# Performance work log

Measured on AMD Instinct MI355X. Metric: run time of the kernel, lower is better.

## Reference

```python
import jax, jax.numpy as jnp
import numpy as np

NUM_HEADS = 8


def setup_inputs() -> dict:
    key = jax.random.key(0)
    B, T, N, C = 16, 24, 716, 256
    H = NUM_HEADS
    D = C // H
    ks = jax.random.split(key, 14)

    def w(k, shape, scale=0.02):
        return jax.random.normal(k, shape, dtype=jnp.float32) * scale

    return {
        "x": jax.random.normal(ks[0], (B, T, N, C), dtype=jnp.float32),
        # nn.Linear weights stored PyTorch-style [out, in]
        "Wq": w(ks[1], (C, C)), "bq": w(ks[2], (C,)),
        "Wk": w(ks[3], (C, C)), "bk": w(ks[4], (C,)),
        "Wv": w(ks[5], (C, C)), "bv": w(ks[6], (C,)),
        "Wo": w(ks[7], (C, C)), "bo": w(ks[8], (C,)),
        # grouped conv1d (kernel_size=1) weights, squeezed: [out_ch, in_ch_per_group]
        "w1": w(ks[9], (C, D)), "b1": w(ks[10], (C,)),
        "w2": w(ks[11], (3 * C, D)), "b2": w(ks[12], (3 * C,)),
    }


def reference(x, Wq, bq, Wk, bk, Wv, bv, Wo, bo, w1, b1, w2, b2):
    B, T, N, C = x.shape
    H = NUM_HEADS
    D = C // H
    BT = B * T
    scale = D ** -0.5

    xf = x.reshape(BT, N, C)
    # q, k, v: [BT, H, N, D]
    q = (xf @ Wq.T + bq).reshape(BT, N, H, D).transpose(0, 2, 1, 3)
    k = (xf @ Wk.T + bk).reshape(BT, N, H, D).transpose(0, 2, 1, 3)
    v = (xf @ Wv.T + bv).reshape(BT, N, H, D).transpose(0, 2, 1, 3)

    # linear attention: kv outer-product [BT, H, D, D], scaled by (scale/N)
    kv = jnp.einsum('bhnd,bhne->bhde', k, v) * (scale / N)
    attn = jnp.einsum('bhnd,bhde->bhne', q, kv)
    # mean-pooled correction term
    kmean = k.mean(axis=2)  # [BT, H, D]
    vmean = v.mean(axis=2)  # [BT, H, D]
    qk = jnp.einsum('bhnd,bhd->bhn', q, kmean) * scale  # [BT, H, N]
    xa = attn + (1.0 - qk)[..., None] * vmean[:, :, None, :]
    xa = xa.transpose(0, 2, 1, 3).reshape(BT, N, C)

    # dynamic per-channel 3-tap kernel weights from node-mean features
    m = xf.mean(axis=1).reshape(BT, H, D)  # grouped input [BT, H, D]
    h1 = jnp.einsum('bgi,goi->bgo', m, w1.reshape(H, D, D)) + b1.reshape(H, D)
    h1 = jax.nn.gelu(h1, approximate=False)
    h2 = jnp.einsum('bgi,goi->bgo', h1, w2.reshape(H, 3 * D, D)) + b2.reshape(H, 3 * D)
    rw = h2.reshape(BT, C, 3)  # per-(sample, channel) 3-tap kernel

    # depthwise conv1d over node axis with groups = BT*C (cross-correlation)
    vc = v.transpose(0, 1, 3, 2).reshape(BT, C, N)
    vp = jnp.pad(vc, ((0, 0), (0, 0), (1, 1)))
    res = (rw[:, :, 0:1] * vp[:, :, 0:N]
           + rw[:, :, 1:2] * vp[:, :, 1:N + 1]
           + rw[:, :, 2:3] * vp[:, :, 2:N + 2])  # [BT, C, N]

    out = (xa + res.transpose(0, 2, 1)).reshape(B, T, N, C)
    return out @ Wo.T + bo
```

## Files before the change

kernel.cpp:

```cpp
#include <hip/hip_runtime.h>
#include <hip/hip_bf16.h>
#include <math.h>

typedef __attribute__((ext_vector_type(8))) short short8;
typedef __attribute__((ext_vector_type(4))) short sv4;
typedef __attribute__((ext_vector_type(4))) float f32x4;
typedef unsigned int u32;

#define BT_ 384
#define N_ 716
#define C_ 256
#define H_ 8
#define D_ 32
#define MROWS (BT_ * N_)
#define SCALE_ 0.17677669529663687f
#define INVN_ (1.0f / 716.0f)

__device__ __forceinline__ void gload_lds16(const void* g, void* l) {
    __builtin_amdgcn_global_load_lds(
        (const __attribute__((address_space(1))) u32*)g,
        (__attribute__((address_space(3))) u32*)l, 16, 0, 0);
}

__global__ void prep_weights(const float* __restrict__ Wq, const float* __restrict__ bq,
                             const float* __restrict__ Wk, const float* __restrict__ bk,
                             const float* __restrict__ Wv, const float* __restrict__ bv,
                             const float* __restrict__ Wo,
                             __hip_bfloat16* __restrict__ wqkv, float* __restrict__ bqkv,
                             __hip_bfloat16* __restrict__ wo) {
    int idx = blockIdx.x * 256 + threadIdx.x;
    if (idx < 768 * 256) {
        int o = idx >> 8, c = idx & 255;
        const float* W = (o < 256) ? Wq : ((o < 512) ? Wk : Wv);
        int oo = o & 255;
        wqkv[idx] = __float2bfloat16(W[oo * 256 + c]);
    }
    if (idx < 256 * 256) wo[idx] = __float2bfloat16(Wo[idx]);
    if (idx < 768) bqkv[idx] = (idx < 256) ? bq[idx] : ((idx < 512) ? bk[idx - 256] : bv[idx - 512]);
}

__global__ __launch_bounds__(256)
void convert_x(const float* __restrict__ x, __hip_bfloat16* __restrict__ xb,
               float* __restrict__ msum) {
    int bt = blockIdx.x, chunk = blockIdx.y;
    int t = threadIdx.x;
    int c4 = (t & 63) * 4;
    int r0 = t >> 6;
    size_t base = ((size_t)bt * N_ + (size_t)chunk * 179) * C_;
    float s0 = 0.f, s1 = 0.f, s2 = 0.f, s3 = 0.f;
    for (int r = r0; r < 179; r += 4) {
        float4 f = *(const float4*)&x[base + (size_t)r * C_ + c4];
        union { sv4 v; __hip_bfloat16 h[4]; } u;
        u.h[0] = __float2bfloat16(f.x);
        u.h[1] = __float2bfloat16(f.y);
        u.h[2] = __float2bfloat16(f.z);
        u.h[3] = __float2bfloat16(f.w);
        *(sv4*)&xb[base + (size_t)r * C_ + c4] = u.v;
        s0 += f.x; s1 += f.y; s2 += f.z; s3 += f.w;
    }
    atomicAdd(&msum[bt * C_ + c4 + 0], s0);
    atomicAdd(&msum[bt * C_ + c4 + 1], s1);
    atomicAdd(&msum[bt * C_ + c4 + 2], s2);
    atomicAdd(&msum[bt * C_ + c4 + 3], s3);
}

__global__ __launch_bounds__(256)
void mlp_rw(const float* __restrict__ msum, const float* __restrict__ w1,
            const float* __restrict__ b1, const float* __restrict__ w2,
            const float* __restrict__ b2, float* __restrict__ rw) {
    int bt = blockIdx.x;
    int t = threadIdx.x;
    __shared__ float m_l[256];
    __shared__ float h1_l[256];
    m_l[t] = msum[bt * 256 + t] * INVN_;
    __syncthreads();
    int g = t >> 5;
    float a = b1[t];
    #pragma unroll
    for (int i = 0; i < 32; ++i) a += m_l[g * 32 + i] * w1[t * 32 + i];
    h1_l[t] = 0.5f * a * (1.0f + erff(a * 0.70710678118654752f));
    __syncthreads();
    for (int o = t; o < 768; o += 256) {
        int gg = o / 96;
        float s = b2[o];
        #pragma unroll
        for (int i = 0; i < 32; ++i) s += h1_l[gg * 32 + i] * w2[o * 32 + i];
        rw[bt * 768 + o] = s;
    }
}

template<int NCOLS, bool OUT_BF16>
__global__ __launch_bounds__(256, 2)
void gemm_persist(const __hip_bfloat16* __restrict__ A, const __hip_bfloat16* __restrict__ Bm,
                  const float* __restrict__ bias, void* __restrict__ outp) {
    __shared__ __align__(16) __hip_bfloat16 As[2][64 * 256];
    constexpr int NT = MROWS / 64;
    const int cb = blockIdx.x;
    const int ib = blockIdx.y;
    const int tid = threadIdx.x;
    const int lane = tid & 63;
    const int wave = tid >> 6;
    const int wm = wave & 1;
    const int wn = wave >> 1;
    const int colBase = cb * 128;
    const int l15 = lane & 15, lq = lane >> 4;
    const int lrow2 = lane >> 5;
    const int p = lane & 31;

    auto stageA = [&](int rt, int buf) {
        #pragma unroll
        for (int i = 0; i < 8; ++i) {
            int r = wave * 16 + 2 * i + lrow2;
            const __hip_bfloat16* g = A + ((size_t)rt * 64 + r) * 256 + ((p ^ (r & 7)) * 8);
            gload_lds16(g, &As[buf][(wave * 16 + 2 * i) * 256]);
        }
    };

    stageA(ib, 0);

    short8 bf[4][8];
    #pragma unroll
    for (int n = 0; n < 4; ++n)
        #pragma unroll
        for (int ks = 0; ks < 8; ++ks)
            bf[n][ks] = *(const short8*)&Bm[(size_t)(colBase + wn * 64 + n * 16 + l15) * 256 + ks * 32 + lq * 8];
    float biasr[4];
    #pragma unroll
    for (int n = 0; n < 4; ++n)
        biasr[n] = bias[colBase + wn * 64 + n * 16 + l15];

    asm volatile("s_waitcnt vmcnt(0)" ::: "memory");
    __builtin_amdgcn_s_barrier();

    int buf = 0;
    for (int rt = ib; rt < NT; rt += 256) {
        int rtn = rt + 256;
        if (rtn < NT) stageA(rtn, buf ^ 1);

        f32x4 acc[2][4] = {};
        #pragma unroll
        for (int ks = 0; ks < 8; ++ks) {
            short8 af[2];
            #pragma unroll
            for (int m = 0; m < 2; ++m) {
                int row = wm * 32 + m * 16 + l15;
                af[m] = *(const short8*)&As[buf][row * 256 + (((ks * 4 + lq) ^ (row & 7)) * 8)];
            }
            #pragma unroll
            for (int m = 0; m < 2; ++m)
                #pragma unroll
                for (int n = 0; n < 4; ++n)
                    acc[m][n] = __builtin_amdgcn_mfma_f32_16x16x32_bf16(af[m], bf[n][ks], acc[m][n], 0, 0, 0);
        }
        asm volatile("s_waitcnt lgkmcnt(0)" ::: "memory");
        __builtin_amdgcn_s_barrier();

        if constexpr (OUT_BF16) {
            __hip_bfloat16* Cs = &As[buf][0];
            #pragma unroll
            for (int m = 0; m < 2; ++m)
                #pragma unroll
                for (int n = 0; n < 4; ++n) {
                    int col = wn * 64 + n * 16 + l15;
                    #pragma unroll
                    for (int j = 0; j < 4; ++j)
                        Cs[(wm * 32 + m * 16 + lq * 4 + j) * 136 + col] =
                            __float2bfloat16(acc[m][n][j] + biasr[n]);
                }
            asm volatile("s_waitcnt lgkmcnt(0)" ::: "memory");
            __builtin_amdgcn_s_barrier();
            int row = tid >> 2, cq = tid & 3;
            __hip_bfloat16* og = (__hip_bfloat16*)outp + ((size_t)rt * 64 + row) * NCOLS + colBase;
            #pragma unroll
            for (int i = 0; i < 4; ++i) {
                int col = cq * 8 + i * 32;
                *(short8*)&og[col] = *(const short8*)&Cs[row * 136 + col];
            }
        } else {
            float* Cs = (float*)&As[buf][0];
            #pragma unroll
            for (int m = 0; m < 2; ++m)
                #pragma unroll
                for (int n = 0; n < 4; ++n) {
                    int col = wn * 64 + n * 16 + l15;
                    #pragma unroll
                    for (int j = 0; j < 4; ++j)
                        Cs[(wm * 32 + m * 16 + lq * 4 + j) * 128 + col] = acc[m][n][j] + biasr[n];
                }
            asm volatile("s_waitcnt lgkmcnt(0)" ::: "memory");
            __builtin_amdgcn_s_barrier();
            int row = tid >> 2, cq = tid & 3;
            float* og = (float*)outp + ((size_t)rt * 64 + row) * NCOLS + colBase;
            #pragma unroll
            for (int i = 0; i < 8; ++i) {
                int col = cq * 4 + i * 16;
                *(float4*)&og[col] = *(const float4*)&Cs[row * 128 + col];
            }
        }
        asm volatile("s_waitcnt vmcnt(4) lgkmcnt(0)" ::: "memory");
        __builtin_amdgcn_s_barrier();
        buf ^= 1;
    }
}

__global__ __launch_bounds__(512, 2)
void reduce_kv(const __hip_bfloat16* __restrict__ qkv, __hip_bfloat16* __restrict__ kv2t,
               float* __restrict__ vmeanb) {
    __shared__ __align__(16) __hip_bfloat16 T[512 * 64];
    const int bt = blockIdx.x;
    const int tid = threadIdx.x;
    const int lane = tid & 63;
    const int h = tid >> 6;
    const int l15 = lane & 15, lq = lane >> 4;
    const int co = tid >> 3;
    const int np3 = tid & 7;
    const size_t rowbase = (size_t)bt * N_;

    union S8 { short8 v; unsigned short u[8]; };
    const short8 zero8 = {0, 0, 0, 0, 0, 0, 0, 0};

    auto issue_loads = [&](int n0, S8* A, S8* B) {
        #pragma unroll
        for (int s = 0; s < 4; ++s) {
            int n = n0 + 2 * (np3 + 8 * s);
            A[s].v = (n < N_)     ? *(const short8*)&qkv[(rowbase + n) * 768 + 256 + co * 8] : zero8;
            B[s].v = (n + 1 < N_) ? *(const short8*)&qkv[(rowbase + n + 1) * 768 + 256 + co * 8] : zero8;
        }
    };
    auto write_lds = [&](S8* A, S8* B) {
        #pragma unroll
        for (int s = 0; s < 4; ++s) {
            int r = 2 * (np3 + 8 * s);
            int slotbase = ((r >> 3));
            #pragma unroll
            for (int j = 0; j < 8; ++j) {
                int c = co * 8 + j;
                u32 w = (u32)A[s].u[j] | ((u32)B[s].u[j] << 16);
                int off = c * 64 + ((slotbase ^ (c & 7)) << 3) + (r & 7);
                *(u32*)&T[off] = w;
            }
        }
    };

    S8 bufA[4], bufB[4], nxtA[4], nxtB[4];
    issue_loads(0, bufA, bufB);

    f32x4 acc[2][2] = {};
    f32x4 acck[2] = {};
    f32x4 accv[2] = {};
    S8 ones;
    #pragma unroll
    for (int j = 0; j < 8; ++j) ones.u[j] = 0x3F80;

    for (int chunk = 0; chunk < 12; ++chunk) {
        if (chunk < 11) issue_loads((chunk + 1) * 64, nxtA, nxtB);
        write_lds(bufA, bufB);
        __syncthreads();
        #pragma unroll
        for (int nc = 0; nc < 2; ++nc) {
            short8 af[2], bf[2];
            int slot = nc * 4 + lq;
            #pragma unroll
            for (int dh = 0; dh < 2; ++dh) {
                int c = h * 32 + dh * 16 + l15;
                af[dh] = *(const short8*)&T[c * 64 + ((slot ^ (c & 7)) << 3)];
            }
            #pragma unroll
            for (int eh = 0; eh < 2; ++eh) {
                int c = 256 + h * 32 + eh * 16 + l15;
                bf[eh] = *(const short8*)&T[c * 64 + ((slot ^ (c & 7)) << 3)];
            }
            #pragma unroll
            for (int dh = 0; dh < 2; ++dh)
                #pragma unroll
                for (int eh = 0; eh < 2; ++eh)
                    acc[dh][eh] = __builtin_amdgcn_mfma_f32_16x16x32_bf16(af[dh], bf[eh], acc[dh][eh], 0, 0, 0);
            #pragma unroll
            for (int dh = 0; dh < 2; ++dh)
                acck[dh] = __builtin_amdgcn_mfma_f32_16x16x32_bf16(af[dh], ones.v, acck[dh], 0, 0, 0);
            #pragma unroll
            for (int eh = 0; eh < 2; ++eh)
                accv[eh] = __builtin_amdgcn_mfma_f32_16x16x32_bf16(ones.v, bf[eh], accv[eh], 0, 0, 0);
        }
        __syncthreads();
        #pragma unroll
        for (int s = 0; s < 4; ++s) { bufA[s] = nxtA[s]; bufB[s] = nxtB[s]; }
    }

    const int bh = bt * 8 + h;
    #pragma unroll
    for (int eh = 0; eh < 2; ++eh) {
        int e = eh * 16 + l15;
        float vme = accv[eh][0] * INVN_;
        #pragma unroll
        for (int dh = 0; dh < 2; ++dh) {
            union { sv4 v; __hip_bfloat16 x[4]; } o;
            #pragma unroll
            for (int j = 0; j < 4; ++j) {
                float km = acck[dh][j] * INVN_;
                float val = acc[dh][eh][j] * (SCALE_ * INVN_) - SCALE_ * km * vme;
                o.x[j] = __float2bfloat16(val);
            }
            *(sv4*)&kv2t[(size_t)bh * 1024 + e * 32 + dh * 16 + lq * 4] = o.v;
        }
        if (lq == 0) vmeanb[bh * 32 + e] = vme;
    }
}

__global__ __launch_bounds__(256)
void fuse_z2(const __hip_bfloat16* __restrict__ qkv, const __hip_bfloat16* __restrict__ kv2t,
             const float* __restrict__ vmeanb, const float* __restrict__ rw,
             __hip_bfloat16* __restrict__ Z) {
    __shared__ __align__(16) __hip_bfloat16 attn[64][256];
    __shared__ __align__(16) __hip_bfloat16 kvl[8192];
    int bt = blockIdx.x;
    int n0 = blockIdx.y * 64;
    int rows = (N_ - n0 < 64) ? (N_ - n0) : 64;
    int t = threadIdx.x;
    const size_t rowbase = (size_t)bt * N_;

    {
        const __hip_bfloat16* src = kv2t + (size_t)bt * 8192;
        #pragma unroll
        for (int i = 0; i < 4; ++i) {
            int off = (t + i * 256) * 8;
            *(short8*)&kvl[off] = *(const short8*)&src[off];
        }
    }
    __syncthreads();

    {
        int lane = t & 63, wave = t >> 6;
        int l15 = lane & 15, lq = lane >> 4;
        int r0 = wave * 16;
        int gn = n0 + r0 + l15; if (gn > N_ - 1) gn = N_ - 1;
        const __hip_bfloat16* qrow = qkv + (rowbase + gn) * 768;
        #pragma unroll
        for (int h = 0; h < 8; ++h) {
            short8 af = *(const short8*)&qrow[h * 32 + lq * 8];
            #pragma unroll
            for (int half = 0; half < 2; ++half) {
                short8 bfr = *(const short8*)&kvl[h * 1024 + (half * 16 + l15) * 32 + lq * 8];
                f32x4 acc = {};
                acc = __builtin_amdgcn_mfma_f32_16x16x32_bf16(af, bfr, acc, 0, 0, 0);
                int col = h * 32 + half * 16 + l15;
                float vm = vmeanb[bt * 256 + col];
                #pragma unroll
                for (int j = 0; j < 4; ++j)
                    attn[r0 + lq * 4 + j][col] = __float2bfloat16(acc[j] + vm);
            }
        }
    }
    __syncthreads();

    {
        int tr = t >> 5;
        int c8 = (t & 31) * 8;
        float w0[8], w1_[8], w2_[8];
        #pragma unroll
        for (int u = 0; u < 8; ++u) {
            w0[u]  = rw[bt * 768 + (c8 + u) * 3 + 0];
            w1_[u] = rw[bt * 768 + (c8 + u) * 3 + 1];
            w2_[u] = rw[bt * 768 + (c8 + u) * 3 + 2];
        }
        int rbeg = tr * 8;
        if (rbeg < rows) {
            int rend = rbeg + 8; if (rend > rows) rend = rows;
            union U8 { short8 v; __hip_bfloat16 h[8]; };
            auto loadv = [&](int gn, float* dst) {
                if (gn >= 0 && gn < N_) {
                    U8 u; u.v = *(const short8*)&qkv[(rowbase + gn) * 768 + 512 + c8];
                    #pragma unroll
                    for (int uu = 0; uu < 8; ++uu) dst[uu] = __bfloat162float(u.h[uu]);
                } else {
                    #pragma unroll
                    for (int uu = 0; uu < 8; ++uu) dst[uu] = 0.0f;
                }
            };
            float vprev[8], vcur[8], vnext[8];
            loadv(n0 + rbeg - 1, vprev);
            loadv(n0 + rbeg, vcur);
            for (int r = rbeg; r < rend; ++r) {
                int gn = n0 + r;
                loadv(gn + 1, vnext);
                U8 at; at.v = *(const short8*)&attn[r][c8];
                U8 zv;
                #pragma unroll
                for (int u = 0; u < 8; ++u) {
                    float s = __bfloat162float(at.h[u]) + w0[u] * vprev[u]
                              + w1_[u] * vcur[u] + w2_[u] * vnext[u];
                    zv.h[u] = __float2bfloat16(s);
                }
                *(short8*)&Z[(rowbase + gn) * 256 + c8] = zv.v;
                #pragma unroll
                for (int u = 0; u < 8; ++u) { vprev[u] = vcur[u]; vcur[u] = vnext[u]; }
            }
        }
    }
}

extern "C" void kernel_launch(void* const* d_in, const int* in_sizes, int n_in,
                              void* d_out, int out_size, void* d_ws, size_t ws_size,
                              hipStream_t stream) {
    (void)in_sizes; (void)n_in; (void)out_size; (void)ws_size;
    const float* x  = (const float*)d_in[0];
    const float* Wq = (const float*)d_in[1];  const float* bq = (const float*)d_in[2];
    const float* Wk = (const float*)d_in[3];  const float* bk = (const float*)d_in[4];
    const float* Wv = (const float*)d_in[5];  const float* bv = (const float*)d_in[6];
    const float* Wo = (const float*)d_in[7];  const float* bo = (const float*)d_in[8];
    const float* w1 = (const float*)d_in[9];  const float* b1 = (const float*)d_in[10];
    const float* w2 = (const float*)d_in[11]; const float* b2 = (const float*)d_in[12];
    float* out = (float*)d_out;

    char* ws = (char*)d_ws;
    size_t off = 0;
    auto take = [&](size_t bytes) -> char* {
        char* p = ws + off;
        off = (off + bytes + 255) & ~(size_t)255;
        return p;
    };

    __hip_bfloat16* qkv   = (__hip_bfloat16*)take((size_t)MROWS * 768 * 2);
    __hip_bfloat16* xb    = (__hip_bfloat16*)take((size_t)MROWS * 256 * 2);
    __hip_bfloat16* Zbuf  = xb;
    __hip_bfloat16* wqkv  = (__hip_bfloat16*)take(768 * 256 * 2);
    __hip_bfloat16* wo    = (__hip_bfloat16*)take(256 * 256 * 2);
    float* bqkv   = (float*)take(768 * 4);
    float* msum   = (float*)take(384 * 256 * 4);
    float* rw     = (float*)take(384 * 768 * 4);
    __hip_bfloat16* kv2t = (__hip_bfloat16*)take((size_t)384 * 8192 * 2);
    float* vmeanb = (float*)take(384 * 256 * 4);

    hipMemsetAsync(msum, 0, 384 * 256 * 4, stream);

    prep_weights<<<768, 256, 0, stream>>>(Wq, bq, Wk, bk, Wv, bv, Wo, wqkv, bqkv, wo);
    convert_x<<<dim3(384, 4), 256, 0, stream>>>(x, xb, msum);
    mlp_rw<<<384, 256, 0, stream>>>(msum, w1, b1, w2, b2, rw);
    gemm_persist<768, true><<<dim3(6, 256), 256, 0, stream>>>(xb, wqkv, bqkv, qkv);
    reduce_kv<<<384, 512, 0, stream>>>(qkv, kv2t, vmeanb);
    fuse_z2<<<dim3(384, 12), 256, 0, stream>>>(qkv, kv2t, vmeanb, rw, Zbuf);
    gemm_persist<256, false><<<dim3(2, 256), 256, 0, stream>>>(Zbuf, wo, bo, out);
}
```

Before: 578.3 us.

## Remap GEMM blocks per XCD and give each wave full-row 64x32 tiles

Launches the persistent GEMMs on a 1D grid and remaps the block index so that each XCD (L&7) handles a contiguous band of row tiles, with the column blocks for a row tile sharing that XCD. This is meant to improve L2 reuse of the A tiles. Each wave now computes all 64 rows by 32 columns instead of 32x64. That halves the per-wave register B fragments and doubles the A fragment LDS reads. The fp32 output epilogue is split into two 32-row halves with a padded stride of 132, which reduces LDS bank conflicts at the cost of extra barriers.

```diff
diff --git a/kernel.cpp b/kernel.cpp
--- a/kernel.cpp
+++ b/kernel.cpp
@@ -89,19 +89,20 @@
     }
 }
 
-template<int NCOLS, bool OUT_BF16>
+template<int NCOLS, int GRIDX, bool OUT_BF16>
 __global__ __launch_bounds__(256, 2)
 void gemm_persist(const __hip_bfloat16* __restrict__ A, const __hip_bfloat16* __restrict__ Bm,
                   const float* __restrict__ bias, void* __restrict__ outp) {
     __shared__ __align__(16) __hip_bfloat16 As[2][64 * 256];
     constexpr int NT = MROWS / 64;
-    const int cb = blockIdx.x;
-    const int ib = blockIdx.y;
+    const int L = blockIdx.x;
+    const int xcd = L & 7, w = L >> 3;
+    const int cb = w % GRIDX;
+    const int ib = xcd * 32 + w / GRIDX;
     const int tid = threadIdx.x;
     const int lane = tid & 63;
     const int wave = tid >> 6;
-    const int wm = wave & 1;
-    const int wn = wave >> 1;
+    const int wn = wave;
     const int colBase = cb * 128;
     const int l15 = lane & 15, lq = lane >> 4;
     const int lrow2 = lane >> 5;
@@ -118,16 +119,16 @@
 
     stageA(ib, 0);
 
-    short8 bf[4][8];
+    short8 bf[2][8];
     #pragma unroll
-    for (int n = 0; n < 4; ++n)
+    for (int n = 0; n < 2; ++n)
         #pragma unroll
         for (int ks = 0; ks < 8; ++ks)
-            bf[n][ks] = *(const short8*)&Bm[(size_t)(colBase + wn * 64 + n * 16 + l15) * 256 + ks * 32 + lq * 8];
-    float biasr[4];
+            bf[n][ks] = *(const short8*)&Bm[(size_t)(colBase + wn * 32 + n * 16 + l15) * 256 + ks * 32 + lq * 8];
+    float biasr[2];
     #pragma unroll
-    for (int n = 0; n < 4; ++n)
-        biasr[n] = bias[colBase + wn * 64 + n * 16 + l15];
+    for (int n = 0; n < 2; ++n)
+        biasr[n] = bias[colBase + wn * 32 + n * 16 + l15];
 
     asm volatile("s_waitcnt vmcnt(0)" ::: "memory");
     __builtin_amdgcn_s_barrier();
@@ -137,19 +138,19 @@
         int rtn = rt + 256;
         if (rtn < NT) stageA(rtn, buf ^ 1);
 
-        f32x4 acc[2][4] = {};
+        f32x4 acc[4][2] = {};
         #pragma unroll
         for (int ks = 0; ks < 8; ++ks) {
-            short8 af[2];
-            #pragma unroll
-            for (int m = 0; m < 2; ++m) {
-                int row = wm * 32 + m * 16 + l15;
+            short8 af[4];
+            #pragma unroll
+            for (int m = 0; m < 4; ++m) {
+                int row = m * 16 + l15;
                 af[m] = *(const short8*)&As[buf][row * 256 + (((ks * 4 + lq) ^ (row & 7)) * 8)];
             }
             #pragma unroll
-            for (int m = 0; m < 2; ++m)
-                #pragma unroll
-                for (int n = 0; n < 4; ++n)
+            for (int m = 0; m < 4; ++m)
+                #pragma unroll
+                for (int n = 0; n < 2; ++n)
                     acc[m][n] = __builtin_amdgcn_mfma_f32_16x16x32_bf16(af[m], bf[n][ks], acc[m][n], 0, 0, 0);
         }
         asm volatile("s_waitcnt lgkmcnt(0)" ::: "memory");
@@ -158,13 +159,13 @@
         if constexpr (OUT_BF16) {
             __hip_bfloat16* Cs = &As[buf][0];
             #pragma unroll
-            for (int m = 0; m < 2; ++m)
-                #pragma unroll
-                for (int n = 0; n < 4; ++n) {
-                    int col = wn * 64 + n * 16 + l15;
+            for (int m = 0; m < 4; ++m)
+                #pragma unroll
+                for (int n = 0; n < 2; ++n) {
+                    int col = wn * 32 + n * 16 + l15;
                     #pragma unroll
                     for (int j = 0; j < 4; ++j)
-                        Cs[(wm * 32 + m * 16 + lq * 4 + j) * 136 + col] =
+                        Cs[(m * 16 + lq * 4 + j) * 136 + col] =
                             __float2bfloat16(acc[m][n][j] + biasr[n]);
                 }
             asm volatile("s_waitcnt lgkmcnt(0)" ::: "memory");
@@ -179,22 +180,29 @@
         } else {
             float* Cs = (float*)&As[buf][0];
             #pragma unroll
-            for (int m = 0; m < 2; ++m)
-                #pragma unroll
-                for (int n = 0; n < 4; ++n) {
-                    int col = wn * 64 + n * 16 + l15;
+            for (int pp = 0; pp < 2; ++pp) {
+                #pragma unroll
+                for (int mm = 0; mm < 2; ++mm) {
+                    int m = 2 * pp + mm;
                     #pragma unroll
-                    for (int j = 0; j < 4; ++j)
-                        Cs[(wm * 32 + m * 16 + lq * 4 + j) * 128 + col] = acc[m][n][j] + biasr[n];
+                    for (int n = 0; n < 2; ++n) {
+                        int col = wn * 32 + n * 16 + l15;
+                        #pragma unroll
+                        for (int j = 0; j < 4; ++j)
+                            Cs[(mm * 16 + lq * 4 + j) * 132 + col] = acc[m][n][j] + biasr[n];
+                    }
                 }
-            asm volatile("s_waitcnt lgkmcnt(0)" ::: "memory");
-            __builtin_amdgcn_s_barrier();
-            int row = tid >> 2, cq = tid & 3;
-            float* og = (float*)outp + ((size_t)rt * 64 + row) * NCOLS + colBase;
-            #pragma unroll
-            for (int i = 0; i < 8; ++i) {
-                int col = cq * 4 + i * 16;
-                *(float4*)&og[col] = *(const float4*)&Cs[row * 128 + col];
+                asm volatile("s_waitcnt lgkmcnt(0)" ::: "memory");
+                __builtin_amdgcn_s_barrier();
+                int row = tid >> 3, k = tid & 7;
+                float* og = (float*)outp + ((size_t)rt * 64 + pp * 32 + row) * NCOLS + colBase;
+                #pragma unroll
+                for (int i = 0; i < 4; ++i) {
+                    int col = k * 4 + i * 32;
+                    *(float4*)&og[col] = *(const float4*)&Cs[row * 132 + col];
+                }
+                asm volatile("s_waitcnt lgkmcnt(0)" ::: "memory");
+                __builtin_amdgcn_s_barrier();
             }
         }
         asm volatile("s_waitcnt vmcnt(4) lgkmcnt(0)" ::: "memory");
@@ -436,8 +444,8 @@
     prep_weights<<<768, 256, 0, stream>>>(Wq, bq, Wk, bk, Wv, bv, Wo, wqkv, bqkv, wo);
     convert_x<<<dim3(384, 4), 256, 0, stream>>>(x, xb, msum);
     mlp_rw<<<384, 256, 0, stream>>>(msum, w1, b1, w2, b2, rw);
-    gemm_persist<768, true><<<dim3(6, 256), 256, 0, stream>>>(xb, wqkv, bqkv, qkv);
+    gemm_persist<768, 6, true><<<1536, 256, 0, stream>>>(xb, wqkv, bqkv, qkv);
     reduce_kv<<<384, 512, 0, stream>>>(qkv, kv2t, vmeanb);
     fuse_z2<<<dim3(384, 12), 256, 0, stream>>>(qkv, kv2t, vmeanb, rw, Zbuf);
-    gemm_persist<256, false><<<dim3(2, 256), 256, 0, stream>>>(Zbuf, wo, bo, out);
-}
+    gemm_persist<256, 2, false><<<512, 256, 0, stream>>>(Zbuf, wo, bo, out);
+}
```

Result: faster. 543.8 us (-6.0%).
